# Kernel tuning notes

Measured on AMD Instinct MI355X. Metric: run time of the kernel, lower is better.

Reference implementation:

```python
import jax, jax.numpy as jnp
import numpy as np

D_MODEL = 2048
N_HEADS = 16
N_KV_HEADS = 4
DH = D_MODEL // N_HEADS          # 128
GROUPS = N_HEADS // N_KV_HEADS   # 4
ROPE_BASE = 10000.0
B, T = 2, 2048


def _rope_tables(positions):
    # positions: [T] int -> cos,sin [T, DH//2]
    inv = 1.0 / (ROPE_BASE ** (jnp.arange(0, DH, 2, dtype=jnp.float32) / DH))
    ang = positions.astype(jnp.float32)[:, None] * inv[None, :]
    return jnp.cos(ang), jnp.sin(ang)


def _apply_rope(x, cos, sin):
    # x: [B,H,T,DH]; cos/sin: [1,1,T,DH//2]; interleaved even/odd rotation
    even, odd = x[..., ::2], x[..., 1::2]
    xe = even * cos - odd * sin
    xo = even * sin + odd * cos
    return jnp.stack([xe, xo], axis=-1).reshape(x.shape)


def setup_inputs() -> dict:
    key = jax.random.key(0)
    k1, k2, k3 = jax.random.split(key, 3)
    qkv_dim = D_MODEL + 2 * N_KV_HEADS * DH
    x = jax.random.normal(k1, (B, T, D_MODEL), dtype=jnp.float32)
    Wqkv = jax.random.normal(k2, (D_MODEL, qkv_dim), dtype=jnp.float32) / np.sqrt(D_MODEL).astype(np.float32)
    Wo = jax.random.normal(k3, (N_HEADS * DH, D_MODEL), dtype=jnp.float32) / np.sqrt(N_HEADS * DH).astype(np.float32)
    return {"x": x, "Wqkv": Wqkv, "Wo": Wo, "start_pos": 0}


def reference(x, Wqkv, Wo, start_pos):
    Bx, Tx, _ = x.shape
    qkv = x @ Wqkv  # [B,T,D + 2*HKV*DH]
    q, k, v = jnp.split(qkv, [N_HEADS * DH, N_HEADS * DH + N_KV_HEADS * DH], axis=-1)
    q = q.reshape(Bx, Tx, N_HEADS, DH).transpose(0, 2, 1, 3)      # [B,H,T,DH]
    k = k.reshape(Bx, Tx, N_KV_HEADS, DH).transpose(0, 2, 1, 3)   # [B,HKV,T,DH]
    v = v.reshape(Bx, Tx, N_KV_HEADS, DH).transpose(0, 2, 1, 3)

    pos = start_pos + jnp.arange(Tx)
    cos, sin = _rope_tables(pos)
    cos = cos[None, None]; sin = sin[None, None]
    q = _apply_rope(q, cos, sin)
    k = _apply_rope(k, cos, sin)

    # GQA: repeat_interleave kv heads
    k = jnp.repeat(k, GROUPS, axis=1)  # [B,H,T,DH]
    v = jnp.repeat(v, GROUPS, axis=1)

    scale = 1.0 / np.sqrt(DH).astype(np.float32)
    att = jnp.einsum('bhqd,bhkd->bhqk', q, k) * scale
    causal = jnp.triu(jnp.ones((Tx, Tx), dtype=bool), 1)
    att = jnp.where(causal[None, None], jnp.float32(-jnp.inf), att)
    att = jax.nn.softmax(att, axis=-1)
    y = jnp.einsum('bhqk,bhkd->bhqd', att, v)
    y = y.transpose(0, 2, 1, 3).reshape(Bx, Tx, N_HEADS * DH)
    return y @ Wo
```

## Files before the change

### kernel.cpp

```cpp
#include <hip/hip_runtime.h>
#include <math.h>

#define D_MODEL 2048
#define N_HEADS 16
#define N_KV    4
#define DH      128
#define QKV_DIM 3072
#define TT      2048
#define BB      2
#define ROWS    (BB*TT)

#define VS_STRIDE 72
#define PS_STRIDE 72

typedef unsigned short u16;
typedef short short8 __attribute__((ext_vector_type(8)));
typedef short short4v __attribute__((ext_vector_type(4)));
typedef float float4v __attribute__((ext_vector_type(4)));

__device__ inline float b2f(u16 h) {
    union { unsigned u; float f; } v; v.u = ((unsigned)h) << 16; return v.f;
}
__device__ inline u16 f2b(float f) {
    union { float f; unsigned u; } v; v.f = f;
    unsigned r = v.u + 0x7FFF + ((v.u >> 16) & 1);
    return (u16)(r >> 16);
}

__device__ inline void async16(const void* g, void* l) {
    __builtin_amdgcn_global_load_lds(
        (const __attribute__((address_space(1))) void*)g,
        (__attribute__((address_space(3))) void*)l, 16, 0, 0);
}

__global__ void convert_f2b(const float* __restrict__ src, u16* __restrict__ dst) {
    int i = blockIdx.x * 256 + threadIdx.x;
    float4v a = *(const float4v*)(src + (size_t)i * 4);
    short4v p;
    p[0] = (short)f2b(a[0]); p[1] = (short)f2b(a[1]);
    p[2] = (short)f2b(a[2]); p[3] = (short)f2b(a[3]);
    *(short4v*)(dst + (size_t)i * 4) = p;
}

__global__ void transpose_f2b(const float* __restrict__ src, u16* __restrict__ dst,
                              int R, int C, int col0) {
    __shared__ __align__(16) u16 tile[32][33];
    int bc = blockIdx.x * 32, br = blockIdx.y * 32;
    int tx = threadIdx.x & 31, ty = threadIdx.x >> 5;
    for (int i = ty; i < 32; i += 8)
        tile[i][tx] = f2b(src[(size_t)(br + i) * C + col0 + bc + tx]);
    __syncthreads();
    for (int i = ty; i < 32; i += 8)
        dst[(size_t)(bc + i) * R + br + tx] = tile[tx][i];
}

template<bool F32OUT, bool ROPE>
__global__ __launch_bounds__(256) void gemm_bt_async(
    const u16* __restrict__ A, const u16* __restrict__ Bt1, const u16* __restrict__ Bt2,
    int nsplit, void* __restrict__ Cv, int M, int N, int K, const int* __restrict__ sp) {
    __shared__ __align__(16) u16 As[128 * 32];
    __shared__ __align__(16) u16 Bs[128 * 32];
    const int tid = threadIdx.x;
    const int wave = tid >> 6, lane = tid & 63;
    const int quad = lane >> 4, l16 = lane & 15;
    const int bm = blockIdx.y * 128, bn = blockIdx.x * 128;
    const int wm = (wave >> 1) * 64, wn = (wave & 1) * 64;
    const int srow = wave * 32 + (lane >> 2);
    const int scol = (lane & 3) * 8;
    const u16* Bt = (bn < nsplit) ? (Bt1 + (size_t)bn * K)
                                  : (Bt2 + (size_t)(bn - nsplit) * K);

    float4v acc[4][4] = {};

    for (int k0 = 0; k0 < K; k0 += 32) {
        async16(A + (size_t)(bm + srow) * K + k0 + scol, (char*)As + wave * 2048);
        async16(A + (size_t)(bm + srow + 16) * K + k0 + scol, (char*)As + wave * 2048 + 1024);
        async16(Bt + (size_t)srow * K + k0 + scol, (char*)Bs + wave * 2048);
        async16(Bt + (size_t)(srow + 16) * K + k0 + scol, (char*)Bs + wave * 2048 + 1024);
        __syncthreads();
        short8 af[4], bf[4];
#pragma unroll
        for (int i = 0; i < 4; i++)
            af[i] = *(const short8*)(As + (wm + i * 16 + l16) * 32 + quad * 8);
#pragma unroll
        for (int j = 0; j < 4; j++)
            bf[j] = *(const short8*)(Bs + (wn + j * 16 + l16) * 32 + quad * 8);
#pragma unroll
        for (int i = 0; i < 4; i++)
#pragma unroll
            for (int j = 0; j < 4; j++)
                acc[i][j] = __builtin_amdgcn_mfma_f32_16x16x32_bf16(af[i], bf[j], acc[i][j], 0, 0, 0);
        __syncthreads();
    }
    const int sp0 = ROPE ? *sp : 0;
#pragma unroll
    for (int j = 0; j < 4; j++) {
        int col = bn + wn + j * 16 + l16;
        bool do_rope = ROPE && (col < 2560);
        float inv = 0.f;
        if (do_rope) inv = __expf(-0.14391156816f * (float)((col & 127) >> 1));
#pragma unroll
        for (int i = 0; i < 4; i++) {
            int row0 = bm + wm + i * 16 + quad * 4;
#pragma unroll
            for (int r = 0; r < 4; r++) {
                float v = acc[i][j][r];
                if (do_rope) {
                    float partner = __shfl_xor(v, 1, 64);
                    float ang = (float)(sp0 + ((row0 + r) & (TT - 1))) * inv;
                    float c = __cosf(ang), s = __sinf(ang);
                    v = (col & 1) ? (partner * s + v * c)
                                  : (v * c - partner * s);
                }
                if (F32OUT) ((float*)Cv)[(size_t)(row0 + r) * N + col] = v;
                else        ((u16*)Cv)[(size_t)(row0 + r) * N + col] = f2b(v);
            }
        }
    }
}

__global__ __launch_bounds__(256, 2) void attn_kernel(
    const u16* __restrict__ qkv, u16* __restrict__ y) {
    __shared__ __align__(16) u16 Ks[2][64 * 128];
    __shared__ __align__(16) u16 Vs[128 * VS_STRIDE];
    __shared__ __align__(16) u16 Ps[4][32 * PS_STRIDE];

    const int tid = threadIdx.x;
    const int wave = tid >> 6, lane = tid & 63;
    const int quad = lane >> 4, l16 = lane & 15;
    const int bx = blockIdx.x;
    const int xg = bx & 7;
    const int b = xg >> 2, hk = xg & 3;
    const int jj = bx >> 3;
    const int h = hk * 4 + ((jj >> 1) & 3);
    const int s = jj >> 3;
    const int qt = (jj & 1) ? (15 - s) : s;
    const int qcol = h * 128;
    const int kcol = 2048 + hk * 128;
    const int vcol = 2560 + hk * 128;
    const float scale = 0.08838834764831845f;

    const int wq0 = qt * 128 + wave * 32;
    short8 qf[2][4];
#pragma unroll
    for (int g = 0; g < 2; g++) {
        const u16* qrow = qkv + (size_t)(b * TT + wq0 + g * 16 + l16) * QKV_DIM + qcol;
#pragma unroll
        for (int d = 0; d < 4; d++)
            qf[g][d] = *(const short8*)(qrow + d * 32 + quad * 8);
    }

    float4v Oacc[2][8] = {};
    float4v Ol[2] = {};
    const short8 ONES = {(short)0x3F80, (short)0x3F80, (short)0x3F80, (short)0x3F80,
                         (short)0x3F80, (short)0x3F80, (short)0x3F80, (short)0x3F80};

    const int ktmax = 2 * qt + 1;

    size_t kg[4];
#pragma unroll
    for (int si = 0; si < 4; si++) {
        int rl = (si * 4 + quad) & 7;
        kg[si] = (size_t)(wave * 16 + si * 4 + quad) * QKV_DIM
               + (size_t)((l16 ^ rl) * 8);
    }
    {
        const u16* kb = qkv + (size_t)(b * TT) * QKV_DIM;
#pragma unroll
        for (int si = 0; si < 4; si++)
            async16(kb + kcol + kg[si], (char*)Ks[0] + wave * 4096 + si * 1024);
    }
    short8 vreg[4];
#pragma unroll
    for (int si = 0; si < 4; si++)
        vreg[si] = *(const short8*)(qkv + (size_t)(b * TT + lane) * QKV_DIM + vcol + (wave * 4 + si) * 8);

    for (int kt = 0; kt <= ktmax; kt++) {
        const u16* Kcur = Ks[kt & 1];
        __syncthreads();
#pragma unroll
        for (int si = 0; si < 4; si++) {
            int dgi = wave * 4 + si;
#pragma unroll
            for (int j8 = 0; j8 < 8; j8++)
                Vs[(dgi * 8 + j8) * VS_STRIDE + lane] = (u16)vreg[si][j8];
        }
        __syncthreads();
        if (kt < ktmax) {
            const u16* kb = qkv + (size_t)(b * TT + (kt + 1) * 64) * QKV_DIM;
#pragma unroll
            for (int si = 0; si < 4; si++)
                async16(kb + kcol + kg[si], (char*)Ks[(kt + 1) & 1] + wave * 4096 + si * 1024);
#pragma unroll
            for (int si = 0; si < 4; si++)
                vreg[si] = *(const short8*)(kb + (size_t)lane * QKV_DIM + vcol + (wave * 4 + si) * 8);
        }

        float4v S[2][4] = {};
#pragma unroll
        for (int d = 0; d < 4; d++) {
#pragma unroll
            for (int j = 0; j < 4; j++) {
                short8 bk = *(const short8*)(Kcur + (j * 16 + l16) * 128
                                             + (((d * 4 + quad) ^ (l16 & 7)) * 8));
#pragma unroll
                for (int g = 0; g < 2; g++)
                    S[g][j] = __builtin_amdgcn_mfma_f32_16x16x32_bf16(qf[g][d], bk, S[g][j], 0, 0, 0);
            }
        }
        const int kvb = kt * 64 + l16;
        const bool diag = (kt * 64 + 63 > wq0);
#pragma unroll
        for (int g = 0; g < 2; g++) {
            const int qbase = wq0 + g * 16 + quad * 4;
#pragma unroll
            for (int j = 0; j < 4; j++)
#pragma unroll
                for (int r = 0; r < 4; r++) {
                    bool masked = diag && (kvb + j * 16 > qbase + r);
                    float p = masked ? 0.f : __expf(S[g][j][r] * scale);
                    Ps[wave][(g * 16 + quad * 4 + r) * PS_STRIDE + j * 16 + l16] = f2b(p);
                }
        }
        __asm__ volatile("s_waitcnt lgkmcnt(0)" ::: "memory");
#pragma unroll
        for (int ks = 0; ks < 2; ks++) {
            short8 ap[2];
#pragma unroll
            for (int g = 0; g < 2; g++)
                ap[g] = *(const short8*)(Ps[wave] + (g * 16 + l16) * PS_STRIDE + ks * 32 + quad * 8);
#pragma unroll
            for (int dt = 0; dt < 8; dt++) {
                short8 bv = *(const short8*)(Vs + (dt * 16 + l16) * VS_STRIDE + ks * 32 + quad * 8);
#pragma unroll
                for (int g = 0; g < 2; g++)
                    Oacc[g][dt] = __builtin_amdgcn_mfma_f32_16x16x32_bf16(ap[g], bv, Oacc[g][dt], 0, 0, 0);
            }
#pragma unroll
            for (int g = 0; g < 2; g++)
                Ol[g] = __builtin_amdgcn_mfma_f32_16x16x32_bf16(ap[g], ONES, Ol[g], 0, 0, 0);
        }
    }
#pragma unroll
    for (int g = 0; g < 2; g++)
#pragma unroll
        for (int dt = 0; dt < 8; dt++)
#pragma unroll
            for (int r = 0; r < 4; r++) {
                float v = Oacc[g][dt][r] / Ol[g][r];
                y[(size_t)(b * TT + wq0 + g * 16 + quad * 4 + r) * D_MODEL
                  + h * 128 + dt * 16 + l16] = f2b(v);
            }
}

extern "C" void kernel_launch(void* const* d_in, const int* in_sizes, int n_in,
                              void* d_out, int out_size, void* d_ws, size_t ws_size,
                              hipStream_t stream) {
    const float* x    = (const float*)d_in[0];
    const float* Wqkv = (const float*)d_in[1];
    const float* Wo   = (const float*)d_in[2];
    const int*   sp   = (const int*)d_in[3];

    char* ws = (char*)d_ws;
    char* dob = (char*)d_out;
    u16*   xb     = (u16*)ws;
    u16*   Y      = (u16*)ws;
    u16*   WqkvTA = (u16*)(ws + 16777216);
    u16*   WoT    = (u16*)(ws + 16777216);
    u16*   QKV    = (u16*)d_out;
    u16*   WqkvTB = (u16*)(dob + 25165824);
    float* out    = (float*)d_out;

    convert_f2b<<<ROWS * D_MODEL / 4 / 256, 256, 0, stream>>>(x, xb);
    transpose_f2b<<<dim3(64, 64), 256, 0, stream>>>(Wqkv, WqkvTA, D_MODEL, QKV_DIM, 0);
    transpose_f2b<<<dim3(32, 64), 256, 0, stream>>>(Wqkv, WqkvTB, D_MODEL, QKV_DIM, 2048);
    gemm_bt_async<false, true><<<dim3(QKV_DIM / 128, ROWS / 128), 256, 0, stream>>>(
        xb, WqkvTA, WqkvTB, 2048, QKV, ROWS, QKV_DIM, D_MODEL, sp);
    transpose_f2b<<<dim3(64, 64), 256, 0, stream>>>(Wo, WoT, D_MODEL, D_MODEL, 0);
    attn_kernel<<<512, 256, 0, stream>>>(QKV, Y);
    gemm_bt_async<true, false><<<dim3(D_MODEL / 128, ROWS / 128), 256, 0, stream>>>(
        Y, WoT, WoT, D_MODEL, out, ROWS, D_MODEL, D_MODEL, sp);
}
```

Baseline: 353.8 us.

## Write QKV in head-major layout with pre-transposed V for async LDS loads

The QKV GEMM epilogue now scatters its output into per-head contiguous Q and K buffers and a transposed V buffer. The attention kernel can then stream both K and V tiles into double-buffered LDS with async global-to-LDS loads, replacing the register round-trip and per-element LDS transpose of V. P and V LDS tiles switch to XOR-swizzled 64-wide rows instead of padded strides. The trade-off is a scattered, column-strided store pattern for V in the GEMM epilogue and higher LDS use in the attention kernel.

```diff
diff --git a/kernel.cpp b/kernel.cpp
--- a/kernel.cpp
+++ b/kernel.cpp
@@ -10,17 +10,15 @@
 #define BB      2
 #define ROWS    (BB*TT)
 
-#define VS_STRIDE 72
-#define PS_STRIDE 72
+#define QP_OFF 0u
+#define KP_OFF 8388608u
+#define VT_OFF 10485760u
 
 typedef unsigned short u16;
 typedef short short8 __attribute__((ext_vector_type(8)));
 typedef short short4v __attribute__((ext_vector_type(4)));
 typedef float float4v __attribute__((ext_vector_type(4)));
 
-__device__ inline float b2f(u16 h) {
-    union { unsigned u; float f; } v; v.u = ((unsigned)h) << 16; return v.f;
-}
 __device__ inline u16 f2b(float f) {
     union { float f; unsigned u; } v; v.f = f;
     unsigned r = v.u + 0x7FFF + ((v.u >> 16) & 1);
@@ -112,8 +110,23 @@
                     v = (col & 1) ? (partner * s + v * c)
                                   : (v * c - partner * s);
                 }
-                if (F32OUT) ((float*)Cv)[(size_t)(row0 + r) * N + col] = v;
-                else        ((u16*)Cv)[(size_t)(row0 + r) * N + col] = f2b(v);
+                if (F32OUT) {
+                    ((float*)Cv)[(size_t)(row0 + r) * N + col] = v;
+                } else {
+                    int rw = row0 + r;
+                    int bb = rw >> 11, t = rw & 2047;
+                    size_t addr;
+                    if (col < 2048)
+                        addr = QP_OFF + (size_t)(bb * 16 + (col >> 7)) * 262144
+                             + (size_t)t * 128 + (col & 127);
+                    else if (col < 2560)
+                        addr = KP_OFF + (size_t)(bb * 4 + ((col - 2048) >> 7)) * 262144
+                             + (size_t)t * 128 + (col & 127);
+                    else
+                        addr = VT_OFF + (size_t)(bb * 4 + ((col - 2560) >> 7)) * 262144
+                             + (size_t)(col & 127) * 2048 + t;
+                    ((u16*)Cv)[addr] = f2b(v);
+                }
             }
         }
     }
@@ -122,8 +135,8 @@
 __global__ __launch_bounds__(256, 2) void attn_kernel(
     const u16* __restrict__ qkv, u16* __restrict__ y) {
     __shared__ __align__(16) u16 Ks[2][64 * 128];
-    __shared__ __align__(16) u16 Vs[128 * VS_STRIDE];
-    __shared__ __align__(16) u16 Ps[4][32 * PS_STRIDE];
+    __shared__ __align__(16) u16 Vs[2][128 * 64];
+    __shared__ __align__(16) u16 Ps[4][32 * 64];
 
     const int tid = threadIdx.x;
     const int wave = tid >> 6, lane = tid & 63;
@@ -135,19 +148,18 @@
     const int h = hk * 4 + ((jj >> 1) & 3);
     const int s = jj >> 3;
     const int qt = (jj & 1) ? (15 - s) : s;
-    const int qcol = h * 128;
-    const int kcol = 2048 + hk * 128;
-    const int vcol = 2560 + hk * 128;
+    const int g = b * 4 + hk;
     const float scale = 0.08838834764831845f;
 
     const int wq0 = qt * 128 + wave * 32;
+    const u16* qbase = qkv + QP_OFF + (size_t)(b * 16 + h) * 262144;
     short8 qf[2][4];
 #pragma unroll
-    for (int g = 0; g < 2; g++) {
-        const u16* qrow = qkv + (size_t)(b * TT + wq0 + g * 16 + l16) * QKV_DIM + qcol;
+    for (int gi = 0; gi < 2; gi++) {
+        const u16* qrow = qbase + (size_t)(wq0 + gi * 16 + l16) * 128;
 #pragma unroll
         for (int d = 0; d < 4; d++)
-            qf[g][d] = *(const short8*)(qrow + d * 32 + quad * 8);
+            qf[gi][d] = *(const short8*)(qrow + d * 32 + quad * 8);
     }
 
     float4v Oacc[2][8] = {};
@@ -160,41 +172,40 @@
     size_t kg[4];
 #pragma unroll
     for (int si = 0; si < 4; si++) {
-        int rl = (si * 4 + quad) & 7;
-        kg[si] = (size_t)(wave * 16 + si * 4 + quad) * QKV_DIM
-               + (size_t)((l16 ^ rl) * 8);
-    }
-    {
-        const u16* kb = qkv + (size_t)(b * TT) * QKV_DIM;
-#pragma unroll
-        for (int si = 0; si < 4; si++)
-            async16(kb + kcol + kg[si], (char*)Ks[0] + wave * 4096 + si * 1024);
-    }
-    short8 vreg[4];
+        int kr = wave * 16 + si * 4 + quad;
+        kg[si] = (size_t)kr * 128 + (size_t)((l16 ^ (kr & 7)) * 8);
+    }
+    size_t vg[4];
+#pragma unroll
+    for (int si = 0; si < 4; si++) {
+        int vr = wave * 32 + si * 8 + (lane >> 3);
+        vg[si] = (size_t)vr * 2048 + (size_t)(((lane & 7) ^ (lane >> 3)) * 8);
+    }
+    const u16* Kb = qkv + KP_OFF + (size_t)g * 262144;
+    const u16* Vb = qkv + VT_OFF + (size_t)g * 262144;
+
 #pragma unroll
     for (int si = 0; si < 4; si++)
-        vreg[si] = *(const short8*)(qkv + (size_t)(b * TT + lane) * QKV_DIM + vcol + (wave * 4 + si) * 8);
+        async16(Kb + kg[si], (char*)Ks[0] + wave * 4096 + si * 1024);
+#pragma unroll
+    for (int si = 0; si < 4; si++)
+        async16(Vb + vg[si], (char*)Vs[0] + wave * 4096 + si * 1024);
 
     for (int kt = 0; kt <= ktmax; kt++) {
-        const u16* Kcur = Ks[kt & 1];
-        __syncthreads();
-#pragma unroll
-        for (int si = 0; si < 4; si++) {
-            int dgi = wave * 4 + si;
-#pragma unroll
-            for (int j8 = 0; j8 < 8; j8++)
-                Vs[(dgi * 8 + j8) * VS_STRIDE + lane] = (u16)vreg[si][j8];
-        }
+        const int cur = kt & 1;
         __syncthreads();
         if (kt < ktmax) {
-            const u16* kb = qkv + (size_t)(b * TT + (kt + 1) * 64) * QKV_DIM;
 #pragma unroll
             for (int si = 0; si < 4; si++)
-                async16(kb + kcol + kg[si], (char*)Ks[(kt + 1) & 1] + wave * 4096 + si * 1024);
+                async16(Kb + (size_t)(kt + 1) * 8192 + kg[si],
+                        (char*)Ks[cur ^ 1] + wave * 4096 + si * 1024);
 #pragma unroll
             for (int si = 0; si < 4; si++)
-                vreg[si] = *(const short8*)(kb + (size_t)lane * QKV_DIM + vcol + (wave * 4 + si) * 8);
-        }
+                async16(Vb + (size_t)(kt + 1) * 64 + vg[si],
+                        (char*)Vs[cur ^ 1] + wave * 4096 + si * 1024);
+        }
+        const u16* Kcur = Ks[cur];
+        const u16* Vcur = Vs[cur];
 
         float4v S[2][4] = {};
 #pragma unroll
@@ -204,22 +215,24 @@
                 short8 bk = *(const short8*)(Kcur + (j * 16 + l16) * 128
                                              + (((d * 4 + quad) ^ (l16 & 7)) * 8));
 #pragma unroll
-                for (int g = 0; g < 2; g++)
-                    S[g][j] = __builtin_amdgcn_mfma_f32_16x16x32_bf16(qf[g][d], bk, S[g][j], 0, 0, 0);
+                for (int gi = 0; gi < 2; gi++)
+                    S[gi][j] = __builtin_amdgcn_mfma_f32_16x16x32_bf16(qf[gi][d], bk, S[gi][j], 0, 0, 0);
             }
         }
         const int kvb = kt * 64 + l16;
         const bool diag = (kt * 64 + 63 > wq0);
 #pragma unroll
-        for (int g = 0; g < 2; g++) {
-            const int qbase = wq0 + g * 16 + quad * 4;
+        for (int gi = 0; gi < 2; gi++) {
+            const int qbq = wq0 + gi * 16 + quad * 4;
 #pragma unroll
             for (int j = 0; j < 4; j++)
 #pragma unroll
                 for (int r = 0; r < 4; r++) {
-                    bool masked = diag && (kvb + j * 16 > qbase + r);
-                    float p = masked ? 0.f : __expf(S[g][j][r] * scale);
-                    Ps[wave][(g * 16 + quad * 4 + r) * PS_STRIDE + j * 16 + l16] = f2b(p);
+                    bool masked = diag && (kvb + j * 16 > qbq + r);
+                    float p = masked ? 0.f : __expf(S[gi][j][r] * scale);
+                    int rq = gi * 16 + quad * 4 + r;
+                    int ch = (j * 2 + (l16 >> 3)) ^ (rq & 7);
+                    Ps[wave][rq * 64 + ch * 8 + (l16 & 7)] = f2b(p);
                 }
         }
         __asm__ volatile("s_waitcnt lgkmcnt(0)" ::: "memory");
@@ -227,28 +240,30 @@
         for (int ks = 0; ks < 2; ks++) {
             short8 ap[2];
 #pragma unroll
-            for (int g = 0; g < 2; g++)
-                ap[g] = *(const short8*)(Ps[wave] + (g * 16 + l16) * PS_STRIDE + ks * 32 + quad * 8);
+            for (int gi = 0; gi < 2; gi++)
+                ap[gi] = *(const short8*)(Ps[wave] + (gi * 16 + l16) * 64
+                                          + (((ks * 4 + quad) ^ (l16 & 7)) * 8));
 #pragma unroll
             for (int dt = 0; dt < 8; dt++) {
-                short8 bv = *(const short8*)(Vs + (dt * 16 + l16) * VS_STRIDE + ks * 32 + quad * 8);
-#pragma unroll
-                for (int g = 0; g < 2; g++)
-                    Oacc[g][dt] = __builtin_amdgcn_mfma_f32_16x16x32_bf16(ap[g], bv, Oacc[g][dt], 0, 0, 0);
-            }
-#pragma unroll
-            for (int g = 0; g < 2; g++)
-                Ol[g] = __builtin_amdgcn_mfma_f32_16x16x32_bf16(ap[g], ONES, Ol[g], 0, 0, 0);
-        }
-    }
-#pragma unroll
-    for (int g = 0; g < 2; g++)
+                short8 bv = *(const short8*)(Vcur + (dt * 16 + l16) * 64
+                                             + (((ks * 4 + quad) ^ (l16 & 7)) * 8));
+#pragma unroll
+                for (int gi = 0; gi < 2; gi++)
+                    Oacc[gi][dt] = __builtin_amdgcn_mfma_f32_16x16x32_bf16(ap[gi], bv, Oacc[gi][dt], 0, 0, 0);
+            }
+#pragma unroll
+            for (int gi = 0; gi < 2; gi++)
+                Ol[gi] = __builtin_amdgcn_mfma_f32_16x16x32_bf16(ap[gi], ONES, Ol[gi], 0, 0, 0);
+        }
+    }
+#pragma unroll
+    for (int gi = 0; gi < 2; gi++)
 #pragma unroll
         for (int dt = 0; dt < 8; dt++)
 #pragma unroll
             for (int r = 0; r < 4; r++) {
-                float v = Oacc[g][dt][r] / Ol[g][r];
-                y[(size_t)(b * TT + wq0 + g * 16 + quad * 4 + r) * D_MODEL
+                float v = Oacc[gi][dt][r] / Ol[gi][r];
+                y[(size_t)(b * TT + wq0 + gi * 16 + quad * 4 + r) * D_MODEL
                   + h * 128 + dt * 16 + l16] = f2b(v);
             }
 }
@@ -267,7 +282,7 @@
     u16*   Y      = (u16*)ws;
     u16*   WqkvTA = (u16*)(ws + 16777216);
     u16*   WoT    = (u16*)(ws + 16777216);
-    u16*   QKV    = (u16*)d_out;
+    u16*   QKVp   = (u16*)d_out;
     u16*   WqkvTB = (u16*)(dob + 25165824);
     float* out    = (float*)d_out;
 
@@ -275,9 +290,9 @@
     transpose_f2b<<<dim3(64, 64), 256, 0, stream>>>(Wqkv, WqkvTA, D_MODEL, QKV_DIM, 0);
     transpose_f2b<<<dim3(32, 64), 256, 0, stream>>>(Wqkv, WqkvTB, D_MODEL, QKV_DIM, 2048);
     gemm_bt_async<false, true><<<dim3(QKV_DIM / 128, ROWS / 128), 256, 0, stream>>>(
-        xb, WqkvTA, WqkvTB, 2048, QKV, ROWS, QKV_DIM, D_MODEL, sp);
+        xb, WqkvTA, WqkvTB, 2048, QKVp, ROWS, QKV_DIM, D_MODEL, sp);
     transpose_f2b<<<dim3(64, 64), 256, 0, stream>>>(Wo, WoT, D_MODEL, D_MODEL, 0);
-    attn_kernel<<<512, 256, 0, stream>>>(QKV, Y);
+    attn_kernel<<<512, 256, 0, stream>>>(QKVp, Y);
     gemm_bt_async<true, false><<<dim3(D_MODEL / 128, ROWS / 128), 256, 0, stream>>>(
         Y, WoT, WoT, D_MODEL, out, ROWS, D_MODEL, D_MODEL, sp);
 }
```

Measured after the change: 350.9 us. No clear change (-0.8%).
